# Optimization experiments

Measured on AMD Instinct MI355X. Metric: run time of the kernel, lower is better.

Reference implementation:

```python
import jax, jax.numpy as jnp
import numpy as np

E, D_IN, D_OUT, A, R, T = 8, 1024, 1024, 4, 16, 8192


def setup_inputs() -> dict:
    key = jax.random.key(0)
    ks = jax.random.split(key, 6)
    x = jax.random.normal(ks[0], (T, D_IN), jnp.float32)
    weight = jax.random.normal(ks[1], (E, D_IN, D_OUT), jnp.float32) / np.float32(np.sqrt(D_IN))
    # he_uniform-like scale for lora_A; lora_B random (zeros in real init would hide the LoRA path)
    lora_A = jax.random.normal(ks[2], (A, E, D_IN, R), jnp.float32) * np.float32(np.sqrt(2.0 / D_IN))
    lora_B = jax.random.normal(ks[3], (A, E, R, D_OUT), jnp.float32) * np.float32(0.02)
    lora_scaling = jax.random.uniform(ks[4], (A,), jnp.float32, 0.5, 1.5)
    group_sizes = jnp.full((E,), T // E, dtype=jnp.int32)  # sums to T
    adapter_indices_sorted = jax.random.randint(ks[5], (T,), 0, A, dtype=jnp.int32)
    return {
        'x': x, 'weight': weight, 'lora_A': lora_A, 'lora_B': lora_B,
        'lora_scaling': lora_scaling, 'group_sizes': group_sizes,
        'adapter_indices_sorted': adapter_indices_sorted,
    }


def reference(x, weight, lora_A, lora_B, lora_scaling, group_sizes, adapter_indices_sorted):
    total_tokens, d_in = x.shape
    n_experts, _, d_out = weight.shape
    n_adapters, _, _, rank = lora_A.shape
    n_groups = n_adapters * n_experts

    # Base expert-grouped GEMM: x is already sorted by expert via group_sizes.
    base_out = jax.lax.ragged_dot(x, weight, group_sizes)  # [T, d_out]

    # Combined (adapter, expert) group id per token.
    expert_idx = jnp.repeat(jnp.arange(n_experts), group_sizes, total_repeat_length=total_tokens)
    flat_idx = adapter_indices_sorted * n_experts + expert_idx  # [T]

    # prepare_routing: stable sort tokens by combined group id.
    sort_idx = jnp.argsort(flat_idx, stable=True)
    x_sorted = x[sort_idx]
    combined_group_sizes = jnp.zeros((n_groups,), jnp.int32).at[flat_idx].add(1)
    unsort_idx = jnp.argsort(sort_idx)

    # Nested LoRA grouped GEMMs over flattened (adapter, expert) groups.
    lora_A_flat = lora_A.reshape(n_groups, d_in, rank)
    lora_B_flat = lora_B.reshape(n_groups, rank, d_out)
    intermediate = jax.lax.ragged_dot(x_sorted, lora_A_flat, combined_group_sizes)  # [T, rank]
    lora_out_sorted = jax.lax.ragged_dot(intermediate, lora_B_flat, combined_group_sizes)  # [T, d_out]

    lora_out = lora_out_sorted[unsort_idx] * lora_scaling[adapter_indices_sorted, None]
    return base_out + lora_out
```

## Files before the change

### kernel.cpp

```cpp
#include <hip/hip_runtime.h>
#include <hip/hip_bf16.h>
#include <stdint.h>


#define T_TOK 8192
#define DIN   1024
#define DOUT  1024
#define NE    8
#define NA    4
#define RK    16
#define KEXT  1088
#define NOCT  136

typedef __attribute__((ext_vector_type(8))) short short8;
typedef __attribute__((ext_vector_type(4))) float f32x4;

__device__ __forceinline__ ushort f2bf(float f) {
  union { float f; uint32_t i; } v; v.f = f;
  uint32_t x = v.i;
  return (ushort)((x + 0x7fffu + ((x >> 16) & 1u)) >> 16);
}

__device__ __forceinline__ void gload_lds16(const void* g, void* l) {
  __builtin_amdgcn_global_load_lds(
      (const __attribute__((address_space(1))) uint32_t*)g,
      (__attribute__((address_space(3))) uint32_t*)l,
      16, 0, 0);
}

__device__ __forceinline__ int expert_of_row(const int* __restrict__ gs, int row) {
  int cum = 0, e = 0;
#pragma unroll
  for (int i = 0; i < NE; ++i) { if (row >= cum) e = i; cum += gs[i]; }
  return e;
}

__global__ __launch_bounds__(256) void k_prepA(
    const float* __restrict__ lora_A, const float* __restrict__ lora_scaling,
    ushort* __restrict__ Aoct) {
  const int bid = blockIdx.x;
  const int tid = threadIdx.x;
  int u = bid * 4 + (tid >> 6);
  int e = u >> 7, ko = u & 127;
  int c = tid & 63;
  int a = c >> 4, r = c & 15;
  float s = lora_scaling[a];
  ushort o8[8];
#pragma unroll
  for (int j = 0; j < 8; ++j) {
    float v = lora_A[((size_t)(a * NE + e) * DIN + ko * 8 + j) * RK + r];
    o8[j] = f2bf(s * v);
  }
  *(uint4*)(Aoct + ((size_t)((e * 128 + ko) * 64 + c)) * 8) = *(const uint4*)o8;
}

__global__ __launch_bounds__(256) void k_main(
    const float* __restrict__ x, ushort* __restrict__ xp,
    const ushort* __restrict__ Aoct,
    const float* __restrict__ weight, const float* __restrict__ lora_B,
    ushort* __restrict__ Boct,
    const int* __restrict__ gs, const int* __restrict__ adapter_idx) {
  __shared__ ushort As2[4 * 16 * 64];
  __shared__ ushort Bs2[4 * 8 * 64 * 8];

  const int bid = blockIdx.x;
  const int tid = threadIdx.x;

  if (bid < 512) {
    const int lane = tid & 63;
    const int wave = tid >> 6;
    const int rows0 = bid * 16;
    const int e = expert_of_row(gs, rows0);
    const ushort* aoct = Aoct + (size_t)e * 128 * 64 * 8;

    const int row = tid >> 4;
    const int seg = tid & 15;
    const int r7 = row & 7;
    const int t4 = seg >> 2;
    const int c0 = (seg & 3) * 2;

    f32x4 acc = (f32x4){0.f, 0.f, 0.f, 0.f};

    for (int it = 0; it < 4; ++it) {
#pragma unroll
      for (int i = 0; i < 8; ++i) {
        int t = i >> 1;
        int o = wave * 2 + (i & 1);
        const ushort* src = aoct + ((size_t)((it * 4 + t) * 8 + o) * 64 + lane) * 8;
        gload_lds16(src, &Bs2[((t * 8 + o) * 64) * 8]);
      }

      const float* srcx = x + (size_t)(rows0 + row) * DIN + it * 256 + seg * 16;
      float4 q0 = ((const float4*)srcx)[0];
      float4 q1 = ((const float4*)srcx)[1];
      float4 q2 = ((const float4*)srcx)[2];
      float4 q3 = ((const float4*)srcx)[3];
      ushort o16[16];
      o16[0]  = f2bf(q0.x); o16[1]  = f2bf(q0.y); o16[2]  = f2bf(q0.z); o16[3]  = f2bf(q0.w);
      o16[4]  = f2bf(q1.x); o16[5]  = f2bf(q1.y); o16[6]  = f2bf(q1.z); o16[7]  = f2bf(q1.w);
      o16[8]  = f2bf(q2.x); o16[9]  = f2bf(q2.y); o16[10] = f2bf(q2.z); o16[11] = f2bf(q2.w);
      o16[12] = f2bf(q3.x); o16[13] = f2bf(q3.y); o16[14] = f2bf(q3.z); o16[15] = f2bf(q3.w);

      ushort* dstg = xp + (size_t)(rows0 + row) * KEXT + it * 256 + seg * 16;
      *(uint4*)(dstg)     = ((const uint4*)o16)[0];
      *(uint4*)(dstg + 8) = ((const uint4*)o16)[1];

      *(uint4*)&As2[(t4 * 16 + row) * 64 + ((c0 ^ r7) * 8)]       = ((const uint4*)o16)[0];
      *(uint4*)&As2[(t4 * 16 + row) * 64 + (((c0 + 1) ^ r7) * 8)] = ((const uint4*)o16)[1];

      __syncthreads();

      int m = lane & 15;
#pragma unroll
      for (int t = 0; t < 4; ++t) {
#pragma unroll
        for (int h = 0; h < 2; ++h) {
          int kblk = h * 4 + (lane >> 4);
          short8 af = *(const short8*)&As2[(t * 16 + m) * 64 + (kblk ^ (m & 7)) * 8];
          short8 bfv = *(const short8*)&Bs2[((t * 8 + kblk) * 64 + wave * 16 + m) * 8];
          acc = __builtin_amdgcn_mfma_f32_16x16x32_bf16(af, bfv, acc, 0, 0, 0);
        }
      }
      __syncthreads();
    }

#pragma unroll
    for (int i = 0; i < 4; ++i) {
      int grow = rows0 + (lane >> 4) * 4 + i;
      int a_row = adapter_idx[grow];
      float val = (a_row == wave) ? acc[i] : 0.f;
      xp[(size_t)grow * KEXT + DIN + wave * 16 + (lane & 15)] = f2bf(val);
    }
  } else {
    int e, ko;
    const float* srcbase = nullptr;
    if (bid < 1536) {
      int u = bid - 512;
      e = u >> 7; ko = u & 127;
      srcbase = weight + (size_t)e * DIN * DOUT + (size_t)(ko * 8) * DOUT;
    } else {
      int u = bid - 1536;
      e = u >> 3; int o = u & 7; ko = 128 + o;
    }
    int n4 = tid * 4;
    float v[8][4];
    if (bid < 1536) {
#pragma unroll
      for (int j = 0; j < 8; ++j) {
        float4 q = *(const float4*)(srcbase + (size_t)j * DOUT + n4);
        v[j][0] = q.x; v[j][1] = q.y; v[j][2] = q.z; v[j][3] = q.w;
      }
    } else {
      int o = ko - 128;
#pragma unroll
      for (int j = 0; j < 8; ++j) {
        int kv = o * 8 + j;
        int a = kv >> 4, r = kv & 15;
        float4 q = *(const float4*)(lora_B + (size_t)((a * NE + e) * RK + r) * DOUT + n4);
        v[j][0] = q.x; v[j][1] = q.y; v[j][2] = q.z; v[j][3] = q.w;
      }
    }
    ushort* dst = Boct + ((size_t)(e * NOCT + ko) * DOUT + n4) * 8;
#pragma unroll
    for (int i = 0; i < 4; ++i) {
      ushort o8[8];
#pragma unroll
      for (int j = 0; j < 8; ++j) o8[j] = f2bf(v[j][i]);
      *(uint4*)(dst + i * 8) = *(const uint4*)o8;
    }
  }
}

__global__ __launch_bounds__(256) void k_gemm(
    const ushort* __restrict__ xp, const ushort* __restrict__ Boct,
    const int* __restrict__ gs, float* __restrict__ out) {
  __shared__ ushort As[128 * 64];
  __shared__ ushort Bs[8 * 128 * 8];

  const int tid = threadIdx.x;
  const int lane = tid & 63;
  const int wave = tid >> 6;
  const int wm = wave >> 1, wn = wave & 1;

  const int bid = blockIdx.x;
  const int swz = (bid & 7) * 64 + (bid >> 3);
  const int row0 = (swz >> 3) * 128;
  const int n0 = (swz & 7) * 128;
  const int e = expert_of_row(gs, row0);
  const ushort* boct = Boct + (size_t)e * NOCT * DOUT * 8;

  f32x4 acc[4][4];
#pragma unroll
  for (int mi = 0; mi < 4; ++mi)
#pragma unroll
    for (int ni = 0; ni < 4; ++ni) acc[mi][ni] = (f32x4){0.f, 0.f, 0.f, 0.f};

  const int r8 = lane >> 3;
  const int c8s = (lane & 7) ^ r8;

  for (int kt = 0; kt < 17; ++kt) {
#pragma unroll
    for (int rd = 0; rd < 4; ++rd) {
      int r = wave * 32 + rd * 8 + r8;
      const ushort* src = xp + (size_t)(row0 + r) * KEXT + kt * 64 + c8s * 8;
      gload_lds16(src, &As[(wave * 32 + rd * 8) * 64]);
    }
#pragma unroll
    for (int rd = 0; rd < 4; ++rd) {
      int u = wave * 4 + rd;
      int o = u >> 1, hf = u & 1;
      const ushort* src = boct + ((size_t)(kt * 8 + o) * DOUT + n0 + hf * 64 + lane) * 8;
      gload_lds16(src, &Bs[(o * 128 + hf * 64) * 8]);
    }
    __syncthreads();

#pragma unroll
    for (int h = 0; h < 2; ++h) {
      int kblk = h * 4 + (lane >> 4);
      short8 af[4], bfv[4];
#pragma unroll
      for (int mi = 0; mi < 4; ++mi) {
        int m = wm * 64 + mi * 16 + (lane & 15);
        af[mi] = *(const short8*)&As[m * 64 + (kblk ^ (m & 7)) * 8];
      }
#pragma unroll
      for (int ni = 0; ni < 4; ++ni) {
        int n = wn * 64 + ni * 16 + (lane & 15);
        bfv[ni] = *(const short8*)&Bs[(kblk * 128 + n) * 8];
      }
#pragma unroll
      for (int mi = 0; mi < 4; ++mi)
#pragma unroll
        for (int ni = 0; ni < 4; ++ni)
          acc[mi][ni] = __builtin_amdgcn_mfma_f32_16x16x32_bf16(
              af[mi], bfv[ni], acc[mi][ni], 0, 0, 0);
    }
    __syncthreads();
  }

#pragma unroll
  for (int mi = 0; mi < 4; ++mi) {
#pragma unroll
    for (int ni = 0; ni < 4; ++ni) {
      int col = n0 + wn * 64 + ni * 16 + (lane & 15);
#pragma unroll
      for (int i = 0; i < 4; ++i) {
        int r = row0 + wm * 64 + mi * 16 + (lane >> 4) * 4 + i;
        out[(size_t)r * DOUT + col] = acc[mi][ni][i];
      }
    }
  }
}

extern "C" void kernel_launch(void* const* d_in, const int* in_sizes, int n_in,
                              void* d_out, int out_size, void* d_ws, size_t ws_size,
                              hipStream_t stream) {
  const float* x            = (const float*)d_in[0];
  const float* weight       = (const float*)d_in[1];
  const float* lora_A       = (const float*)d_in[2];
  const float* lora_B       = (const float*)d_in[3];
  const float* lora_scaling = (const float*)d_in[4];
  const int*   group_sizes  = (const int*)d_in[5];
  const int*   adapter_idx  = (const int*)d_in[6];
  float* out = (float*)d_out;

  const size_t sz_xp    = (size_t)T_TOK * KEXT * 2;
  const size_t sz_boct  = (size_t)NE * NOCT * DOUT * 8 * 2;
  ushort* xp   = (ushort*)d_ws;
  ushort* boct = (ushort*)((char*)d_ws + sz_xp);
  ushort* aoct = (ushort*)((char*)d_ws + sz_xp + sz_boct);

  k_prepA<<<256, 256, 0, stream>>>(lora_A, lora_scaling, aoct);
  k_main<<<1600, 256, 0, stream>>>(x, xp, aoct, weight, lora_B, boct,
                                   group_sizes, adapter_idx);
  k_gemm<<<512, 256, 0, stream>>>(xp, boct, group_sizes, out);
}
```

Measured before the change: 156.3 us.

## Drop bf16 x staging buffer; convert x inside GEMM and store only LoRA intermediate

The first kernel no longer writes a bf16 copy of x into an extended 1088-wide buffer. It writes only the 64-wide scaled LoRA intermediate to a small buffer. The GEMM kernel now reads fp32 x directly, converts it to bf16 into LDS in each K tile, and finishes with an extra K tile that multiplies the intermediate by the LoRA B rows. This removes a write and re-read of about 17MB of bf16 activations, but the GEMM now reads fp32 x (double the bytes per tile) through registers instead of direct-to-LDS loads, and the per-tile conversion lands on the GEMM's critical path. It also swizzles the first kernel's row-block order.

```diff
diff --git a/kernel.cpp b/kernel.cpp
--- a/kernel.cpp
+++ b/kernel.cpp
@@ -9,7 +9,6 @@
 #define NE    8
 #define NA    4
 #define RK    16
-#define KEXT  1088
 #define NOCT  136
 
 typedef __attribute__((ext_vector_type(8))) short short8;
@@ -54,8 +53,8 @@
   *(uint4*)(Aoct + ((size_t)((e * 128 + ko) * 64 + c)) * 8) = *(const uint4*)o8;
 }
 
-__global__ __launch_bounds__(256) void k_main(
-    const float* __restrict__ x, ushort* __restrict__ xp,
+__global__ __launch_bounds__(256) void k_pv(
+    const float* __restrict__ x, ushort* __restrict__ vs,
     const ushort* __restrict__ Aoct,
     const float* __restrict__ weight, const float* __restrict__ lora_B,
     ushort* __restrict__ Boct,
@@ -67,9 +66,10 @@
   const int tid = threadIdx.x;
 
   if (bid < 512) {
+    const int vb = (bid & 7) * 64 + (bid >> 3);
     const int lane = tid & 63;
     const int wave = tid >> 6;
-    const int rows0 = bid * 16;
+    const int rows0 = vb * 16;
     const int e = expert_of_row(gs, rows0);
     const ushort* aoct = Aoct + (size_t)e * 128 * 64 * 8;
 
@@ -101,10 +101,6 @@
       o16[8]  = f2bf(q2.x); o16[9]  = f2bf(q2.y); o16[10] = f2bf(q2.z); o16[11] = f2bf(q2.w);
       o16[12] = f2bf(q3.x); o16[13] = f2bf(q3.y); o16[14] = f2bf(q3.z); o16[15] = f2bf(q3.w);
 
-      ushort* dstg = xp + (size_t)(rows0 + row) * KEXT + it * 256 + seg * 16;
-      *(uint4*)(dstg)     = ((const uint4*)o16)[0];
-      *(uint4*)(dstg + 8) = ((const uint4*)o16)[1];
-
       *(uint4*)&As2[(t4 * 16 + row) * 64 + ((c0 ^ r7) * 8)]       = ((const uint4*)o16)[0];
       *(uint4*)&As2[(t4 * 16 + row) * 64 + (((c0 + 1) ^ r7) * 8)] = ((const uint4*)o16)[1];
 
@@ -129,7 +125,7 @@
       int grow = rows0 + (lane >> 4) * 4 + i;
       int a_row = adapter_idx[grow];
       float val = (a_row == wave) ? acc[i] : 0.f;
-      xp[(size_t)grow * KEXT + DIN + wave * 16 + (lane & 15)] = f2bf(val);
+      vs[(size_t)grow * 64 + wave * 16 + (lane & 15)] = f2bf(val);
     }
   } else {
     int e, ko;
@@ -171,8 +167,9 @@
   }
 }
 
-__global__ __launch_bounds__(256) void k_gemm(
-    const ushort* __restrict__ xp, const ushort* __restrict__ Boct,
+__global__ __launch_bounds__(256) void k_gemm2(
+    const float* __restrict__ x, const ushort* __restrict__ vs,
+    const ushort* __restrict__ Boct,
     const int* __restrict__ gs, float* __restrict__ out) {
   __shared__ ushort As[128 * 64];
   __shared__ ushort Bs[8 * 128 * 8];
@@ -189,6 +186,10 @@
   const int e = expert_of_row(gs, row0);
   const ushort* boct = Boct + (size_t)e * NOCT * DOUT * 8;
 
+  const int xrow = tid >> 1;
+  const int xseg = tid & 1;
+  const int xr7 = xrow & 7;
+
   f32x4 acc[4][4];
 #pragma unroll
   for (int mi = 0; mi < 4; ++mi)
@@ -198,13 +199,12 @@
   const int r8 = lane >> 3;
   const int c8s = (lane & 7) ^ r8;
 
-  for (int kt = 0; kt < 17; ++kt) {
-#pragma unroll
-    for (int rd = 0; rd < 4; ++rd) {
-      int r = wave * 32 + rd * 8 + r8;
-      const ushort* src = xp + (size_t)(row0 + r) * KEXT + kt * 64 + c8s * 8;
-      gload_lds16(src, &As[(wave * 32 + rd * 8) * 64]);
-    }
+  for (int kt = 0; kt < 16; ++kt) {
+    const float* srcx = x + (size_t)(row0 + xrow) * DIN + kt * 64 + xseg * 32;
+    float4 q[8];
+#pragma unroll
+    for (int j = 0; j < 8; ++j) q[j] = ((const float4*)srcx)[j];
+
 #pragma unroll
     for (int rd = 0; rd < 4; ++rd) {
       int u = wave * 4 + rd;
@@ -212,6 +212,16 @@
       const ushort* src = boct + ((size_t)(kt * 8 + o) * DOUT + n0 + hf * 64 + lane) * 8;
       gload_lds16(src, &Bs[(o * 128 + hf * 64) * 8]);
     }
+
+#pragma unroll
+    for (int i = 0; i < 4; ++i) {
+      ushort o8[8];
+#pragma unroll
+      for (int j = 0; j < 8; ++j)
+        o8[j] = f2bf(((const float*)&q[i * 2 + (j >> 2)])[j & 3]);
+      int c = xseg * 4 + i;
+      *(uint4*)&As[xrow * 64 + ((c ^ xr7) * 8)] = *(const uint4*)o8;
+    }
     __syncthreads();
 
 #pragma unroll
@@ -236,6 +246,45 @@
               af[mi], bfv[ni], acc[mi][ni], 0, 0, 0);
     }
     __syncthreads();
+  }
+
+  {
+#pragma unroll
+    for (int rd = 0; rd < 4; ++rd) {
+      int r = wave * 32 + rd * 8 + r8;
+      const ushort* src = vs + (size_t)(row0 + r) * 64 + c8s * 8;
+      gload_lds16(src, &As[(wave * 32 + rd * 8) * 64]);
+    }
+#pragma unroll
+    for (int rd = 0; rd < 4; ++rd) {
+      int u = wave * 4 + rd;
+      int o = u >> 1, hf = u & 1;
+      const ushort* src = boct + ((size_t)(16 * 8 + o) * DOUT + n0 + hf * 64 + lane) * 8;
+      gload_lds16(src, &Bs[(o * 128 + hf * 64) * 8]);
+    }
+    __syncthreads();
+
+#pragma unroll
+    for (int h = 0; h < 2; ++h) {
+      int kblk = h * 4 + (lane >> 4);
+      short8 af[4], bfv[4];
+#pragma unroll
+      for (int mi = 0; mi < 4; ++mi) {
+        int m = wm * 64 + mi * 16 + (lane & 15);
+        af[mi] = *(const short8*)&As[m * 64 + (kblk ^ (m & 7)) * 8];
+      }
+#pragma unroll
+      for (int ni = 0; ni < 4; ++ni) {
+        int n = wn * 64 + ni * 16 + (lane & 15);
+        bfv[ni] = *(const short8*)&Bs[(kblk * 128 + n) * 8];
+      }
+#pragma unroll
+      for (int mi = 0; mi < 4; ++mi)
+#pragma unroll
+        for (int ni = 0; ni < 4; ++ni)
+          acc[mi][ni] = __builtin_amdgcn_mfma_f32_16x16x32_bf16(
+              af[mi], bfv[ni], acc[mi][ni], 0, 0, 0);
+    }
   }
 
 #pragma unroll
@@ -264,14 +313,14 @@
   const int*   adapter_idx  = (const int*)d_in[6];
   float* out = (float*)d_out;
 
-  const size_t sz_xp    = (size_t)T_TOK * KEXT * 2;
-  const size_t sz_boct  = (size_t)NE * NOCT * DOUT * 8 * 2;
-  ushort* xp   = (ushort*)d_ws;
-  ushort* boct = (ushort*)((char*)d_ws + sz_xp);
-  ushort* aoct = (ushort*)((char*)d_ws + sz_xp + sz_boct);
+  const size_t sz_vs   = (size_t)T_TOK * 64 * 2;
+  const size_t sz_boct = (size_t)NE * NOCT * DOUT * 8 * 2;
+  ushort* vsb  = (ushort*)d_ws;
+  ushort* boct = (ushort*)((char*)d_ws + sz_vs);
+  ushort* aoct = (ushort*)((char*)d_ws + sz_vs + sz_boct);
 
   k_prepA<<<256, 256, 0, stream>>>(lora_A, lora_scaling, aoct);
-  k_main<<<1600, 256, 0, stream>>>(x, xp, aoct, weight, lora_B, boct,
-                                   group_sizes, adapter_idx);
-  k_gemm<<<512, 256, 0, stream>>>(xp, boct, group_sizes, out);
-}
+  k_pv<<<1600, 256, 0, stream>>>(x, vsb, aoct, weight, lora_B, boct,
+                                 group_sizes, adapter_idx);
+  k_gemm2<<<512, 256, 0, stream>>>(x, vsb, boct, group_sizes, out);
+}
```

Measured after the change: 175.4 us. 1.12x slower.
